# Kernel tuning notes

Hardware: AMD Instinct MI355X
Metric: run time of the kernel (lower is better)

## Reference

```python
import jax, jax.numpy as jnp
import numpy as np

LN_EPS = 1e-4
NEG = -1e10


def setup_inputs() -> dict:
    key = jax.random.key(0)
    ks = jax.random.split(key, 5)
    b, p, d, i, h, m = 2, 2048, 1024, 16, 64, 4096
    sd = 1.0 / np.sqrt(d)
    return {
        "x": jax.random.normal(ks[0], (b, p, d), jnp.float32),
        "W_K": jax.random.normal(ks[1], (i, h, d), jnp.float32) * sd,
        "W_Q": jax.random.normal(ks[2], (i, h, d), jnp.float32) * sd,
        "W_V": jax.random.normal(ks[3], (i, h, d), jnp.float32) * sd,
        "w_ln": jnp.ones((d,), jnp.float32),
        "b_ln": jnp.zeros((d,), jnp.float32),
        "W_in": jax.random.normal(ks[4], (m, d), jnp.float32) * sd,
        "b_in": jnp.zeros((m,), jnp.float32),
        "W_out": jax.random.normal(jax.random.fold_in(key, 9), (d, m), jnp.float32) * sd,
        "b_out": jnp.zeros((d,), jnp.float32),
    }


def reference(x, W_K, W_Q, W_V, w_ln, b_ln, W_in, b_in, W_out, b_out):
    b, p, d = x.shape
    # --- attention (unscaled softmax, scaled=False in TransformerBlock) ---
    k = jnp.einsum('ihd,bpd->biph', W_K, x)
    q = jnp.einsum('ihd,bpd->biph', W_Q, x)
    v = jnp.einsum('ihd,bpd->biph', W_V, x)
    scores = jnp.einsum('biph,biqh->biqp', k, q)  # [b,i,q_pos,k_pos]
    causal = jnp.tril(jnp.ones((p, p), bool))      # k_pos <= q_pos
    masked = jnp.where(causal, scores, NEG)
    attn = jax.nn.softmax(masked, axis=-1)
    z = jnp.einsum('biph,biqp->biqh', v, attn)     # [b,i,q,h]
    z_flat = jnp.transpose(z, (0, 2, 1, 3)).reshape(b, p, d)  # b q (i h)
    x = x + z_flat
    # --- custom LayerNorm: unbiased std, eps added to std ---
    c = x - jnp.mean(x, axis=-1, keepdims=True)
    std = jnp.sqrt(jnp.sum(c * c, axis=-1, keepdims=True) / (d - 1))
    x = c / (std + LN_EPS) * w_ln + b_ln
    # --- MLP with residual ---
    hpre = jnp.einsum('md,bpd->bpm', W_in, x) + b_in
    hact = jax.nn.gelu(hpre, approximate=False)
    mlp = jnp.einsum('dm,bpm->bpd', W_out, hact) + b_out
    return x + mlp
```

## Files before the change

kernel.cpp:

```cpp
#include <hip/hip_runtime.h>
#include <hip/hip_bf16.h>

typedef __bf16 bf16x8 __attribute__((ext_vector_type(8)));
typedef float f32x4 __attribute__((ext_vector_type(4)));

#define BAR() __builtin_amdgcn_s_barrier()
#define MEMFENCE() asm volatile("" ::: "memory")
#define LGKM0() asm volatile("s_waitcnt lgkmcnt(0)" ::: "memory")
#define VMCNT8() asm volatile("s_waitcnt vmcnt(8)" ::: "memory")
#define VMCNT6() asm volatile("s_waitcnt vmcnt(6)" ::: "memory")
#define VMCNT2() asm volatile("s_waitcnt vmcnt(2)" ::: "memory")
#define VMCNT0() asm volatile("s_waitcnt vmcnt(0)" ::: "memory")

__device__ __forceinline__ void gload_lds16(const void* g, void* l) {
  __builtin_amdgcn_global_load_lds(
      (const __attribute__((address_space(1))) void*)g,
      (__attribute__((address_space(3))) void*)l, 16, 0, 0);
}

__device__ __forceinline__ float fast_erf(float x) {
  float xa = fabsf(x);
  float t = __builtin_amdgcn_rcpf(1.f + 0.3275911f * xa);
  float poly = t * (0.254829592f +
              t * (-0.284496736f +
              t * (1.421413741f +
              t * (-1.453152027f + t * 1.061405429f))));
  float e = poly * __expf(-xa * xa);
  return x >= 0.f ? 1.f - e : e - 1.f;
}

__global__ __launch_bounds__(256) void k_f2b_all(
    const float* __restrict__ x, const float* __restrict__ wk,
    const float* __restrict__ wq, const float* __restrict__ wv,
    const float* __restrict__ wi, const float* __restrict__ wo,
    __bf16* __restrict__ xb, __bf16* __restrict__ wqkv,
    __bf16* __restrict__ winb, __bf16* __restrict__ woutb) {
  int i = (blockIdx.x * 256 + threadIdx.x) * 4;
  const float* s; __bf16* d; int off;
  if (i < 4194304)       { s = x;  d = xb;             off = i; }
  else if (i < 5242880)  { s = wk; d = wqkv;           off = i - 4194304; }
  else if (i < 6291456)  { s = wq; d = wqkv + 1048576; off = i - 5242880; }
  else if (i < 7340032)  { s = wv; d = wqkv + 2097152; off = i - 6291456; }
  else if (i < 11534336) { s = wi; d = winb;           off = i - 7340032; }
  else                   { s = wo; d = woutb;          off = i - 11534336; }
  const float4 v = *(const float4*)(s + off);
  d[off + 0] = (__bf16)v.x;
  d[off + 1] = (__bf16)v.y;
  d[off + 2] = (__bf16)v.z;
  d[off + 3] = (__bf16)v.w;
}

template <int EPI, int WM, int WN, int MI, int NI, int SMT, int SNT>
__global__ __launch_bounds__(WM * WN * 64, 2) void k_gemm(
    const __bf16* __restrict__ A, const __bf16* __restrict__ B, int N, int K,
    int NT, const float* __restrict__ bias, const float* __restrict__ resid,
    float* __restrict__ outf, __bf16* __restrict__ outb,
    __bf16* __restrict__ ok, __bf16* __restrict__ oq, __bf16* __restrict__ ovt) {
  constexpr int BM = WM * MI * 16, BN = WN * NI * 16;
  constexpr int LA = BM / (8 * WM * WN);
  constexpr int LB = BN / (8 * WM * WN);
  __shared__ __align__(16) __bf16 lds[2][(BM + BN) * 64];
  const int tid = threadIdx.x;
  const int lane = tid & 63, wid = tid >> 6;
  const int wr = wid / WN, wc = wid % WN;
  const int lr = lane & 15, lh = lane >> 4;
  const int bid = blockIdx.x;
  const int cpx = gridDim.x >> 3;
  const int sid = (bid & 7) * cpx + (bid >> 3);
  const int stn = NT / SNT;
  const int stile = sid / (SMT * SNT);
  const int within = sid - stile * (SMT * SNT);
  const int mt = (stile / stn) * SMT + within / SNT;
  const int nt = (stile % stn) * SNT + within % SNT;
  const int m0 = mt * BM, n0 = nt * BN;
  const int nkt = K >> 6;

  const __bf16* aSrc[LA]; int aDst[LA];
  const __bf16* bSrc[LB]; int bDst[LB];
#pragma unroll
  for (int j = 0; j < LA; ++j) {
    int chunk = (wid * LA + j) * 64 + lane;
    int row = chunk >> 3, c8 = chunk & 7;
    int g8 = c8 ^ (row & 7);
    aSrc[j] = A + (size_t)(m0 + row) * K + g8 * 8;
    aDst[j] = chunk * 8;
  }
#pragma unroll
  for (int j = 0; j < LB; ++j) {
    int chunk = (wid * LB + j) * 64 + lane;
    int row = chunk >> 3, c8 = chunk & 7;
    int g8 = c8 ^ (row & 7);
    bSrc[j] = B + (size_t)(n0 + row) * K + g8 * 8;
    bDst[j] = chunk * 8;
  }

  auto stage = [&](int t, int bufi) {
    const int k0 = t << 6;
    __bf16* As = lds[bufi];
    __bf16* Bs = lds[bufi] + BM * 64;
#pragma unroll
    for (int j = 0; j < LA; ++j) gload_lds16(aSrc[j] + k0, As + aDst[j]);
#pragma unroll
    for (int j = 0; j < LB; ++j) gload_lds16(bSrc[j] + k0, Bs + bDst[j]);
  };

  int aOff[2][MI], bOff[2][NI];
#pragma unroll
  for (int ks = 0; ks < 2; ++ks) {
#pragma unroll
    for (int mi = 0; mi < MI; ++mi) {
      int row = wr * (MI * 16) + mi * 16 + lr;
      aOff[ks][mi] = row * 64 + (((ks * 4 + lh) ^ (row & 7)) * 8);
    }
#pragma unroll
    for (int ni = 0; ni < NI; ++ni) {
      int row = wc * (NI * 16) + ni * 16 + lr;
      bOff[ks][ni] = row * 64 + (((ks * 4 + lh) ^ (row & 7)) * 8);
    }
  }

  f32x4 acc[MI][NI] = {};
  stage(0, 0);
  stage(1, 1);
  if constexpr (LA + LB == 8) { VMCNT8(); } else { VMCNT6(); }
  BAR();

  for (int t = 0; t < nkt; ++t) {
    const __bf16* As = lds[t & 1];
    const __bf16* Bs = lds[t & 1] + BM * 64;
    bf16x8 af[2][MI], bf[2][NI];
#pragma unroll
    for (int ks = 0; ks < 2; ++ks) {
#pragma unroll
      for (int mi = 0; mi < MI; ++mi)
        af[ks][mi] = *(const bf16x8*)&As[aOff[ks][mi]];
#pragma unroll
      for (int ni = 0; ni < NI; ++ni)
        bf[ks][ni] = *(const bf16x8*)&Bs[bOff[ks][ni]];
    }
#pragma unroll
    for (int mi = 0; mi < MI; ++mi)
#pragma unroll
      for (int ni = 0; ni < NI; ++ni)
        acc[mi][ni] = __builtin_amdgcn_mfma_f32_16x16x32_bf16(
            af[0][mi], bf[0][ni], acc[mi][ni], 0, 0, 0);
    LGKM0();
    MEMFENCE();
    BAR();
    if (t + 2 < nkt) stage(t + 2, t & 1);
#pragma unroll
    for (int mi = 0; mi < MI; ++mi)
#pragma unroll
      for (int ni = 0; ni < NI; ++ni)
        acc[mi][ni] = __builtin_amdgcn_mfma_f32_16x16x32_bf16(
            af[1][mi], bf[1][ni], acc[mi][ni], 0, 0, 0);
    if (t + 2 < nkt) {
      if constexpr (LA + LB == 8) { VMCNT8(); } else { VMCNT6(); }
    } else {
      VMCNT0();
    }
    MEMFENCE();
    BAR();
  }

#pragma unroll
  for (int mi = 0; mi < MI; ++mi) {
#pragma unroll
    for (int j = 0; j < 4; ++j) {
      const int row = m0 + wr * (MI * 16) + mi * 16 + lh * 4 + j;
#pragma unroll
      for (int ni = 0; ni < NI; ++ni) {
        const int col = n0 + wc * (NI * 16) + ni * 16 + lr;
        float v = acc[mi][ni][j];
        if constexpr (EPI == 0) {
          const int which = col >> 10, c = col & 1023;
          const int ih = c >> 6, hh = c & 63;
          const int bb = row >> 11, pp = row & 2047;
          const int bi = bb * 16 + ih;
          if (which == 0)
            ok[((size_t)bi * 2048 + pp) * 64 + hh] = (__bf16)v;
          else if (which == 1)
            oq[((size_t)bi * 2048 + pp) * 64 + hh] = (__bf16)v;
          else
            ovt[((size_t)bi * 64 + hh) * 2048 + pp] = (__bf16)v;
        } else if constexpr (EPI == 1) {
          float h = v + bias[col];
          float g = 0.5f * h * (1.f + fast_erf(h * 0.70710678118f));
          outb[(size_t)row * N + col] = (__bf16)g;
        } else {
          outf[(size_t)row * N + col] = v + bias[col] + resid[(size_t)row * N + col];
        }
      }
    }
  }
}

__global__ __launch_bounds__(512) void k_attn(const __bf16* __restrict__ kb,
                                              const __bf16* __restrict__ qb,
                                              const __bf16* __restrict__ vt,
                                              float* __restrict__ z) {
  const int tid = threadIdx.x;
  const int lane = tid & 63, w = tid >> 6;
  const int lr = lane & 15, lh = lane >> 4;
  const int wgid = blockIdx.x;
  const int xcd = wgid & 7;
  const int t = wgid >> 3;
  const int c = 15 - (t >> 2);
  const int bi = xcd + 8 * (t & 3);
  const int b = bi >> 4, ih = bi & 15;
  const int qw = c * 128 + w * 16;
  const __bf16* kbase = kb + (size_t)bi * 2048 * 64;
  const __bf16* qbase = qb + (size_t)bi * 2048 * 64;
  const __bf16* vbase = vt + (size_t)bi * 64 * 2048;

  __shared__ __align__(16) __bf16 kv[2][2][64 * 64];
  __shared__ __align__(16) __bf16 plds[8][16 * 76];

  const int nk = 2 * c + 2;

  auto stage = [&](int kt, int bufi) {
    const int k0 = kt << 6;
    const int row = tid >> 3, c8 = tid & 7;
    const int g8 = c8 ^ (row & 7);
    gload_lds16(kbase + (size_t)(k0 + row) * 64 + g8 * 8,
                &kv[bufi][0][tid * 8]);
    gload_lds16(vbase + (size_t)row * 2048 + k0 + g8 * 8,
                &kv[bufi][1][tid * 8]);
  };

  bf16x8 aq[2];
#pragma unroll
  for (int ks = 0; ks < 2; ++ks)
    aq[ks] = *(const bf16x8*)(qbase + (size_t)(qw + lr) * 64 + ks * 32 + lh * 8);

  f32x4 o[4] = {};
  float lsum[4] = {0.f, 0.f, 0.f, 0.f};

  stage(0, 0);
  stage(1, 1);
  VMCNT2();
  BAR();

  for (int kt = 0; kt < nk; ++kt) {
    const int k0 = kt << 6;
    const __bf16* Ks = kv[kt & 1][0];
    const __bf16* Vs = kv[kt & 1][1];
    const bool act = (k0 <= qw + 15);

    if (act) {
      bf16x8 bk[4][2];
#pragma unroll
      for (int n = 0; n < 4; ++n) {
        int r = n * 16 + lr;
#pragma unroll
        for (int ks = 0; ks < 2; ++ks)
          bk[n][ks] = *(const bf16x8*)&Ks[r * 64 + (((ks * 4 + lh) ^ (r & 7)) * 8)];
      }
      f32x4 s[4] = {};
#pragma unroll
      for (int ks = 0; ks < 2; ++ks)
#pragma unroll
        for (int n = 0; n < 4; ++n)
          s[n] = __builtin_amdgcn_mfma_f32_16x16x32_bf16(aq[ks], bk[n][ks], s[n], 0, 0, 0);

      bf16x8 bv[4][2];
#pragma unroll
      for (int ht = 0; ht < 4; ++ht) {
        int r = ht * 16 + lr;
#pragma unroll
        for (int ks = 0; ks < 2; ++ks)
          bv[ht][ks] = *(const bf16x8*)&Vs[r * 64 + (((ks * 4 + lh) ^ (r & 7)) * 8)];
      }

      if (k0 + 63 > qw) {
#pragma unroll
        for (int n = 0; n < 4; ++n)
#pragma unroll
          for (int j = 0; j < 4; ++j) {
            int qpos = qw + lh * 4 + j;
            int kpos = k0 + n * 16 + lr;
            if (kpos > qpos) s[n][j] = -1e10f;
          }
      }

#pragma unroll
      for (int n = 0; n < 4; ++n)
#pragma unroll
        for (int j = 0; j < 4; ++j) s[n][j] = __expf(s[n][j]);
#pragma unroll
      for (int j = 0; j < 4; ++j)
        lsum[j] += (s[0][j] + s[1][j]) + (s[2][j] + s[3][j]);

#pragma unroll
      for (int n = 0; n < 4; ++n)
#pragma unroll
        for (int j = 0; j < 4; ++j)
          plds[w][(lh * 4 + j) * 76 + n * 16 + lr] = (__bf16)s[n][j];
      bf16x8 pa[2];
#pragma unroll
      for (int ks = 0; ks < 2; ++ks)
        pa[ks] = *(const bf16x8*)&plds[w][lr * 76 + ks * 32 + lh * 8];
#pragma unroll
      for (int ks = 0; ks < 2; ++ks)
#pragma unroll
        for (int ht = 0; ht < 4; ++ht)
          o[ht] = __builtin_amdgcn_mfma_f32_16x16x32_bf16(pa[ks], bv[ht][ks], o[ht], 0, 0, 0);
    }

    MEMFENCE();
    BAR();
    if (kt + 2 < nk) {
      stage(kt + 2, kt & 1);
      VMCNT2();
    } else {
      VMCNT0();
    }
    BAR();
  }

#pragma unroll
  for (int m = 1; m < 16; m <<= 1)
#pragma unroll
    for (int j = 0; j < 4; ++j) lsum[j] += __shfl_xor(lsum[j], m);

  float* zr = z + (size_t)b * 2048 * 1024;
#pragma unroll
  for (int j = 0; j < 4; ++j) {
    float inv = 1.f / lsum[j];
    int q = qw + lh * 4 + j;
#pragma unroll
    for (int ht = 0; ht < 4; ++ht)
      zr[(size_t)q * 1024 + ih * 64 + ht * 16 + lr] = o[ht][j] * inv;
  }
}

__global__ __launch_bounds__(256) void k_ln(const float* __restrict__ x,
                                            const float* __restrict__ z,
                                            const float* __restrict__ wln,
                                            const float* __restrict__ bln,
                                            float* __restrict__ y,
                                            __bf16* __restrict__ yb) {
  const int row = blockIdx.x;
  const int t = threadIdx.x;
  const int lane = t & 63, wid = t >> 6;
  const float4 xv = ((const float4*)(x + (size_t)row * 1024))[t];
  const float4 zv = ((const float4*)(z + (size_t)row * 1024))[t];
  float v0 = xv.x + zv.x, v1 = xv.y + zv.y, v2 = xv.z + zv.z, v3 = xv.w + zv.w;
  __shared__ float red[4];
  float s = v0 + v1 + v2 + v3;
#pragma unroll
  for (int m = 1; m < 64; m <<= 1) s += __shfl_xor(s, m);
  if (lane == 0) red[wid] = s;
  __syncthreads();
  const float mean = (red[0] + red[1] + red[2] + red[3]) * (1.f / 1024.f);
  const float c0 = v0 - mean, c1 = v1 - mean, c2 = v2 - mean, c3 = v3 - mean;
  float ss = c0 * c0 + c1 * c1 + c2 * c2 + c3 * c3;
#pragma unroll
  for (int m = 1; m < 64; m <<= 1) ss += __shfl_xor(ss, m);
  __syncthreads();
  if (lane == 0) red[wid] = ss;
  __syncthreads();
  const float var = (red[0] + red[1] + red[2] + red[3]) * (1.f / 1023.f);
  const float inv = 1.f / (sqrtf(var) + 1e-4f);
  const float4 wv = ((const float4*)wln)[t];
  const float4 bv = ((const float4*)bln)[t];
  float y0 = c0 * inv * wv.x + bv.x;
  float y1 = c1 * inv * wv.y + bv.y;
  float y2 = c2 * inv * wv.z + bv.z;
  float y3 = c3 * inv * wv.w + bv.w;
  float4 yo; yo.x = y0; yo.y = y1; yo.z = y2; yo.w = y3;
  ((float4*)(y + (size_t)row * 1024))[t] = yo;
  __bf16* yd = yb + (size_t)row * 1024 + t * 4;
  yd[0] = (__bf16)y0; yd[1] = (__bf16)y1; yd[2] = (__bf16)y2; yd[3] = (__bf16)y3;
}

extern "C" void kernel_launch(void* const* d_in, const int* in_sizes, int n_in,
                              void* d_out, int out_size, void* d_ws, size_t ws_size,
                              hipStream_t stream) {
  const float* x = (const float*)d_in[0];
  const float* W_K = (const float*)d_in[1];
  const float* W_Q = (const float*)d_in[2];
  const float* W_V = (const float*)d_in[3];
  const float* w_ln = (const float*)d_in[4];
  const float* b_ln = (const float*)d_in[5];
  const float* W_in = (const float*)d_in[6];
  const float* b_in = (const float*)d_in[7];
  const float* W_out = (const float*)d_in[8];
  const float* b_out = (const float*)d_in[9];
  float* out = (float*)d_out;

  char* ws = (char*)d_ws;
  const size_t NEEDED = 132120576;
  if (ws_size < NEEDED) return;

  __bf16* xb   = (__bf16*)(ws);
  __bf16* wqkv = (__bf16*)(ws + 8388608);
  __bf16* winb = (__bf16*)(ws + 14680064);
  __bf16* woutb= (__bf16*)(ws + 23068672);
  __bf16* kbuf = (__bf16*)(ws + 31457280);
  __bf16* qbuf = (__bf16*)(ws + 39845888);
  __bf16* vtb  = (__bf16*)(ws + 48234496);
  float*  zb   = (float*)(ws + 56623104);
  float*  yf   = (float*)(ws + 73400320);
  __bf16* ybb  = (__bf16*)(ws + 90177536);
  __bf16* hact = (__bf16*)(ws + 98566144);

  k_f2b_all<<<15360, 256, 0, stream>>>(x, W_K, W_Q, W_V, W_in, W_out,
                                       xb, wqkv, winb, woutb);

  k_gemm<0, 2, 2, 4, 4, 4, 4><<<768, 256, 0, stream>>>(
      xb, wqkv, 3072, 1024, 24, nullptr, nullptr, nullptr, nullptr,
      kbuf, qbuf, vtb);
  k_attn<<<dim3(512), 512, 0, stream>>>(kbuf, qbuf, vtb, zb);
  k_ln<<<4096, 256, 0, stream>>>(x, zb, w_ln, b_ln, yf, ybb);
  k_gemm<1, 2, 2, 4, 4, 4, 4><<<1024, 256, 0, stream>>>(
      ybb, winb, 4096, 1024, 32, b_in, nullptr, nullptr, hact,
      nullptr, nullptr, nullptr);
  k_gemm<2, 2, 2, 4, 2, 2, 2><<<512, 256, 0, stream>>>(
      hact, woutb, 1024, 4096, 16, b_out, yf, out, nullptr,
      nullptr, nullptr, nullptr);
}
```

Before: 189.7 us.

## Add 256x256-tile 8-wave GEMM kernel for QKV and MLP-in projections

```diff
diff --git a/kernel.cpp b/kernel.cpp
--- a/kernel.cpp
+++ b/kernel.cpp
@@ -9,6 +9,7 @@
 #define LGKM0() asm volatile("s_waitcnt lgkmcnt(0)" ::: "memory")
 #define VMCNT8() asm volatile("s_waitcnt vmcnt(8)" ::: "memory")
 #define VMCNT6() asm volatile("s_waitcnt vmcnt(6)" ::: "memory")
+#define VMCNT4() asm volatile("s_waitcnt vmcnt(4)" ::: "memory")
 #define VMCNT2() asm volatile("s_waitcnt vmcnt(2)" ::: "memory")
 #define VMCNT0() asm volatile("s_waitcnt vmcnt(0)" ::: "memory")
 
@@ -50,12 +51,191 @@
   d[off + 3] = (__bf16)v.w;
 }
 
+template <int EPI>
+__global__ __launch_bounds__(512) void k_g8(
+    const __bf16* __restrict__ A, const __bf16* __restrict__ B, int N, int K,
+    int NT, int SMT, int SNT, const float* __restrict__ bias,
+    float* __restrict__ outf, __bf16* __restrict__ outb,
+    __bf16* __restrict__ ok, __bf16* __restrict__ oq, __bf16* __restrict__ ovt) {
+  __shared__ __align__(16) __bf16 lds8[2][32768];
+  const int tid = threadIdx.x;
+  const int lane = tid & 63, wid = tid >> 6;
+  const int wm = wid >> 2, wn = wid & 3;
+  const int lr = lane & 15, lh = lane >> 4;
+  const int bid = blockIdx.x;
+  const int cpx = gridDim.x >> 3;
+  const int sid = (bid & 7) * cpx + (bid >> 3);
+  const int stn = NT / SNT;
+  const int stile = sid / (SMT * SNT);
+  const int within = sid - stile * (SMT * SNT);
+  const int mt = (stile / stn) * SMT + within / SNT;
+  const int nt = (stile % stn) * SNT + within % SNT;
+  const int m0 = mt * 256, n0 = nt * 256;
+  const int nkt = K >> 6;
+
+  const __bf16* aS[4]; int aD[4];
+  const __bf16* bS[4]; int bD[4];
+#pragma unroll
+  for (int h = 0; h < 2; ++h)
+#pragma unroll
+    for (int jj = 0; jj < 2; ++jj) {
+      int chunk = (wid * 2 + jj) * 64 + lane;
+      int rl = chunk >> 3, c8 = chunk & 7;
+      int g8 = c8 ^ (rl & 7);
+      aS[h * 2 + jj] = A + (size_t)(m0 + h * 128 + rl) * K + g8 * 8;
+      aD[h * 2 + jj] = h * 8192 + chunk * 8;
+      bS[h * 2 + jj] = B + (size_t)(n0 + h * 128 + rl) * K + g8 * 8;
+      bD[h * 2 + jj] = 16384 + h * 8192 + chunk * 8;
+    }
+
+  auto stageA = [&](int t) {
+    const int k0 = t << 6;
+    __bf16* L = lds8[t & 1];
+#pragma unroll
+    for (int j = 0; j < 4; ++j) gload_lds16(aS[j] + k0, L + aD[j]);
+  };
+  auto stageBH = [&](int t, int h) {
+    const int k0 = t << 6;
+    __bf16* L = lds8[t & 1];
+#pragma unroll
+    for (int jj = 0; jj < 2; ++jj)
+      gload_lds16(bS[h * 2 + jj] + k0, L + bD[h * 2 + jj]);
+  };
+
+  const int swz0 = ((0 * 4 + lh) ^ (lr & 7)) * 8;
+  const int swz1 = ((1 * 4 + lh) ^ (lr & 7)) * 8;
+
+  f32x4 acc[8][4] = {};
+
+  stageA(0); stageBH(0, 0); stageBH(0, 1);
+  stageBH(1, 0); stageBH(1, 1);
+  VMCNT4();
+  MEMFENCE(); BAR();
+
+  for (int t = 0; t < nkt; ++t) {
+    const __bf16* La = lds8[t & 1];
+    const __bf16* Lb = lds8[t & 1] + 16384;
+    bf16x8 bfr[2][4];
+    bf16x8 af[2][2];
+
+#pragma unroll
+    for (int ni = 0; ni < 4; ++ni) {
+      int r = wn * 64 + ni * 16 + lr;
+      bfr[0][ni] = *(const bf16x8*)&Lb[r * 64 + swz0];
+      bfr[1][ni] = *(const bf16x8*)&Lb[r * 64 + swz1];
+    }
+#pragma unroll
+    for (int ii = 0; ii < 2; ++ii) {
+      int r = wm * 128 + ii * 16 + lr;
+      af[ii][0] = *(const bf16x8*)&La[r * 64 + swz0];
+      af[ii][1] = *(const bf16x8*)&La[r * 64 + swz1];
+    }
+    if (t + 1 < nkt) stageA(t + 1);
+    MEMFENCE(); BAR();
+    __builtin_amdgcn_s_setprio(1);
+#pragma unroll
+    for (int ii = 0; ii < 2; ++ii)
+#pragma unroll
+      for (int ni = 0; ni < 4; ++ni) {
+        acc[ii][ni] = __builtin_amdgcn_mfma_f32_16x16x32_bf16(af[ii][0], bfr[0][ni], acc[ii][ni], 0, 0, 0);
+        acc[ii][ni] = __builtin_amdgcn_mfma_f32_16x16x32_bf16(af[ii][1], bfr[1][ni], acc[ii][ni], 0, 0, 0);
+      }
+    __builtin_amdgcn_s_setprio(0);
+    MEMFENCE(); BAR();
+
+#pragma unroll
+    for (int ii = 0; ii < 2; ++ii) {
+      int r = wm * 128 + (2 + ii) * 16 + lr;
+      af[ii][0] = *(const bf16x8*)&La[r * 64 + swz0];
+      af[ii][1] = *(const bf16x8*)&La[r * 64 + swz1];
+    }
+    if (t + 2 < nkt) stageBH(t + 2, 0);
+    MEMFENCE(); BAR();
+    __builtin_amdgcn_s_setprio(1);
+#pragma unroll
+    for (int ii = 0; ii < 2; ++ii)
+#pragma unroll
+      for (int ni = 0; ni < 4; ++ni) {
+        acc[2 + ii][ni] = __builtin_amdgcn_mfma_f32_16x16x32_bf16(af[ii][0], bfr[0][ni], acc[2 + ii][ni], 0, 0, 0);
+        acc[2 + ii][ni] = __builtin_amdgcn_mfma_f32_16x16x32_bf16(af[ii][1], bfr[1][ni], acc[2 + ii][ni], 0, 0, 0);
+      }
+    __builtin_amdgcn_s_setprio(0);
+    MEMFENCE(); BAR();
+
+#pragma unroll
+    for (int ii = 0; ii < 2; ++ii) {
+      int r = wm * 128 + (4 + ii) * 16 + lr;
+      af[ii][0] = *(const bf16x8*)&La[r * 64 + swz0];
+      af[ii][1] = *(const bf16x8*)&La[r * 64 + swz1];
+    }
+    if (t + 2 < nkt) stageBH(t + 2, 1);
+    MEMFENCE(); BAR();
+    __builtin_amdgcn_s_setprio(1);
+#pragma unroll
+    for (int ii = 0; ii < 2; ++ii)
+#pragma unroll
+      for (int ni = 0; ni < 4; ++ni) {
+        acc[4 + ii][ni] = __builtin_amdgcn_mfma_f32_16x16x32_bf16(af[ii][0], bfr[0][ni], acc[4 + ii][ni], 0, 0, 0);
+        acc[4 + ii][ni] = __builtin_amdgcn_mfma_f32_16x16x32_bf16(af[ii][1], bfr[1][ni], acc[4 + ii][ni], 0, 0, 0);
+      }
+    __builtin_amdgcn_s_setprio(0);
+    MEMFENCE(); BAR();
+
+#pragma unroll
+    for (int ii = 0; ii < 2; ++ii) {
+      int r = wm * 128 + (6 + ii) * 16 + lr;
+      af[ii][0] = *(const bf16x8*)&La[r * 64 + swz0];
+      af[ii][1] = *(const bf16x8*)&La[r * 64 + swz1];
+    }
+    MEMFENCE(); BAR();
+    __builtin_amdgcn_s_setprio(1);
+#pragma unroll
+    for (int ii = 0; ii < 2; ++ii)
+#pragma unroll
+      for (int ni = 0; ni < 4; ++ni) {
+        acc[6 + ii][ni] = __builtin_amdgcn_mfma_f32_16x16x32_bf16(af[ii][0], bfr[0][ni], acc[6 + ii][ni], 0, 0, 0);
+        acc[6 + ii][ni] = __builtin_amdgcn_mfma_f32_16x16x32_bf16(af[ii][1], bfr[1][ni], acc[6 + ii][ni], 0, 0, 0);
+      }
+    __builtin_amdgcn_s_setprio(0);
+    if (t + 2 < nkt) { VMCNT4(); } else { VMCNT0(); }
+    MEMFENCE(); BAR();
+  }
+
+#pragma unroll
+  for (int mi = 0; mi < 8; ++mi) {
+#pragma unroll
+    for (int j = 0; j < 4; ++j) {
+      const int row = m0 + wm * 128 + mi * 16 + lh * 4 + j;
+#pragma unroll
+      for (int ni = 0; ni < 4; ++ni) {
+        const int col = n0 + wn * 64 + ni * 16 + lr;
+        float v = acc[mi][ni][j];
+        if constexpr (EPI == 0) {
+          const int which = col >> 10, c = col & 1023;
+          const int ih = c >> 6, hh = c & 63;
+          const int bb2 = row >> 11, pp = row & 2047;
+          const int bi = bb2 * 16 + ih;
+          if (which == 0)
+            ok[((size_t)bi * 2048 + pp) * 64 + hh] = (__bf16)v;
+          else if (which == 1)
+            oq[((size_t)bi * 2048 + pp) * 64 + hh] = (__bf16)v;
+          else
+            ovt[((size_t)bi * 64 + hh) * 2048 + pp] = (__bf16)v;
+        } else {
+          float h = v + bias[col];
+          float g = 0.5f * h * (1.f + fast_erf(h * 0.70710678118f));
+          outb[(size_t)row * N + col] = (__bf16)g;
+        }
+      }
+    }
+  }
+}
+
 template <int EPI, int WM, int WN, int MI, int NI, int SMT, int SNT>
 __global__ __launch_bounds__(WM * WN * 64, 2) void k_gemm(
     const __bf16* __restrict__ A, const __bf16* __restrict__ B, int N, int K,
     int NT, const float* __restrict__ bias, const float* __restrict__ resid,
-    float* __restrict__ outf, __bf16* __restrict__ outb,
-    __bf16* __restrict__ ok, __bf16* __restrict__ oq, __bf16* __restrict__ ovt) {
+    float* __restrict__ outf, __bf16* __restrict__ outb) {
   constexpr int BM = WM * MI * 16, BN = WN * NI * 16;
   constexpr int LA = BM / (8 * WM * WN);
   constexpr int LB = BN / (8 * WM * WN);
@@ -172,23 +352,12 @@
       for (int ni = 0; ni < NI; ++ni) {
         const int col = n0 + wc * (NI * 16) + ni * 16 + lr;
         float v = acc[mi][ni][j];
-        if constexpr (EPI == 0) {
-          const int which = col >> 10, c = col & 1023;
-          const int ih = c >> 6, hh = c & 63;
-          const int bb = row >> 11, pp = row & 2047;
-          const int bi = bb * 16 + ih;
-          if (which == 0)
-            ok[((size_t)bi * 2048 + pp) * 64 + hh] = (__bf16)v;
-          else if (which == 1)
-            oq[((size_t)bi * 2048 + pp) * 64 + hh] = (__bf16)v;
-          else
-            ovt[((size_t)bi * 64 + hh) * 2048 + pp] = (__bf16)v;
+        if constexpr (EPI == 2) {
+          outf[(size_t)row * N + col] = v + bias[col] + resid[(size_t)row * N + col];
         } else if constexpr (EPI == 1) {
           float h = v + bias[col];
           float g = 0.5f * h * (1.f + fast_erf(h * 0.70710678118f));
           outb[(size_t)row * N + col] = (__bf16)g;
-        } else {
-          outf[(size_t)row * N + col] = v + bias[col] + resid[(size_t)row * N + col];
         }
       }
     }
@@ -408,15 +577,12 @@
   k_f2b_all<<<15360, 256, 0, stream>>>(x, W_K, W_Q, W_V, W_in, W_out,
                                        xb, wqkv, winb, woutb);
 
-  k_gemm<0, 2, 2, 4, 4, 4, 4><<<768, 256, 0, stream>>>(
-      xb, wqkv, 3072, 1024, 24, nullptr, nullptr, nullptr, nullptr,
-      kbuf, qbuf, vtb);
+  k_g8<0><<<192, 512, 0, stream>>>(xb, wqkv, 3072, 1024, 12, 4, 4, nullptr,
+                                   nullptr, nullptr, kbuf, qbuf, vtb);
   k_attn<<<dim3(512), 512, 0, stream>>>(kbuf, qbuf, vtb, zb);
   k_ln<<<4096, 256, 0, stream>>>(x, zb, w_ln, b_ln, yf, ybb);
-  k_gemm<1, 2, 2, 4, 4, 4, 4><<<1024, 256, 0, stream>>>(
-      ybb, winb, 4096, 1024, 32, b_in, nullptr, nullptr, hact,
-      nullptr, nullptr, nullptr);
+  k_g8<1><<<256, 512, 0, stream>>>(ybb, winb, 4096, 1024, 16, 4, 4, b_in,
+                                   nullptr, hact, nullptr, nullptr, nullptr);
   k_gemm<2, 2, 2, 4, 2, 2, 2><<<512, 256, 0, stream>>>(
-      hact, woutb, 1024, 4096, 16, b_out, yf, out, nullptr,
-      nullptr, nullptr, nullptr);
-}
+      hact, woutb, 1024, 4096, 16, b_out, yf, out, nullptr);
+}
```

After: 210.1 us. 10.8% more time.
